# Kernel tuning notes

Measured on AMD Instinct MI355X. Metric: run time of the kernel, lower is better.

## Reference

```python
import jax, jax.numpy as jnp
import numpy as np

NUM_FRAMES = 16   # frames gathered per proposal (hardcoded 16 in source)
TOPK = 3          # get_max_score_timestamps uses topk=3


def setup_inputs() -> dict:
    key = jax.random.key(0)
    k0, k1, k2, k3, k4 = jax.random.split(key, 5)
    B, S, N, T, D = 64, 16, 256, 256, 500
    frames_feat = jax.random.normal(k0, (B, T, D), dtype=jnp.float32)
    duration = jax.random.uniform(k1, (B,), minval=30.0, maxval=120.0, dtype=jnp.float32)
    s = jax.random.uniform(k2, (B, S), minval=0.0, maxval=0.8, dtype=jnp.float32) * duration[:, None]
    length = jax.random.uniform(k3, (B, S), minval=0.05, maxval=0.2, dtype=jnp.float32) * duration[:, None]
    e = jnp.minimum(s + length, duration[:, None])
    props = jnp.stack([s, e], axis=-1)          # [B,S,2] (start,end) seconds
    y_t = props[:, :, None, :]                  # [B,S,1,2] gt timestamps
    scores = jax.random.uniform(k4, (B, S, 1, N, N), dtype=jnp.float32)
    return {"frames_feat": frames_feat, "props": props, "duration": duration,
            "y_t": y_t, "scores": scores}


def reference(frames_feat, props, duration, y_t, scores):
    B, T, D = frames_feat.shape
    S = props.shape[1]
    N = scores.shape[-1]

    # ---- _generate_proposals_feat: vectorized per-proposal frame gather ----
    s_fr = jnp.minimum((props[..., 0] / duration[:, None] * T).astype(jnp.int32), T - 1)  # [B,S]
    e_fr = jnp.minimum((props[..., 1] / duration[:, None] * T).astype(jnp.int32), T - 1)
    steps = jnp.arange(NUM_FRAMES, dtype=jnp.float32)
    # np.linspace(s, e, 16, endpoint=False) == s + k*(e-s)/16, then int cast + clamp
    lin = s_fr[..., None].astype(jnp.float32) + steps * (e_fr - s_fr)[..., None].astype(jnp.float32) / NUM_FRAMES
    idx = jnp.minimum(lin.astype(jnp.int32), T - 1)                       # [B,S,16]
    gathered = jnp.take_along_axis(frames_feat[:, None], idx[..., None], axis=2)  # [B,S,16,D]
    zero_prop = (props[..., 0] == 0) & (props[..., 1] == 0) & (duration[:, None] == 0)
    props_feats = jnp.where(zero_prop[..., None, None], 0.0, gathered).reshape(B * S, NUM_FRAMES, D)

    # ---- calculate_overlaps: IoU of all (s_i, e_j) clip pairs vs gt segment ----
    s_times = jnp.arange(N, dtype=jnp.float32) * duration[:, None] / N        # [B,N]
    e_times = jnp.arange(1, N + 1, dtype=jnp.float32) * duration[:, None] / N  # [B,N]
    gt_s = y_t[:, :, 0, 0]   # [B,S]
    gt_e = y_t[:, :, 0, 1]
    ps = s_times[:, None, :, None]                 # [B,1,N,1] pred start (row i)
    pe = e_times[:, None, None, :]                 # [B,1,1,N] pred end   (col j)
    gs = gt_s[:, :, None, None]
    ge = gt_e[:, :, None, None]
    inter = jnp.maximum(0.0, jnp.minimum(pe, ge) - jnp.maximum(ps, gs))
    union = jnp.maximum(0.0, jnp.maximum(pe, ge) - jnp.minimum(ps, gs))
    overlaps = inter / (union + 1e-6)              # [B,S,N,N]
    gt_zero = (gt_s == 0) & (gt_e == 0)
    overlaps = jnp.where(gt_zero[..., None, None], 0.0, overlaps)

    # ---- get_max_score_timestamps: batched top-3 over flattened NxN maps ----
    score_map = scores[:, :, 0]                    # [B,S,N,N]
    flat = score_map.reshape(B, S, N * N)
    top_vals, top_idx = jax.lax.top_k(flat, TOPK)  # [B,S,3]
    pos_i = (top_idx // N).astype(jnp.float32)
    pos_j = (top_idx % N).astype(jnp.float32)
    # target_size = NUM_SAMPLE_CLIPS // TARGET_STRIDE == N here
    ts = jnp.stack([pos_i, pos_j], axis=-1) / N * duration[:, None, None, None]  # [B,S,3,2]
    valid = (flat.sum(-1) > 0.001)[..., None]      # [B,S,1]
    max_scores = jnp.where(valid, top_vals, 0.0)
    max_timestamps = jnp.where(valid[..., None], ts, 0.0)

    return props_feats, overlaps, max_timestamps, max_scores
```

## Files before the change

kernel.cpp:

```cpp
#include <hip/hip_runtime.h>
#include <float.h>

typedef float f32x4 __attribute__((ext_vector_type(4)));

static constexpr long OUT0 = 0;
static constexpr long OUT1 = 8192000;
static constexpr long OUT2 = 75300864;
static constexpr long OUT3 = 75307008;

__global__ __launch_bounds__(256) void propfeat_kernel(
    const float* __restrict__ frames, const float* __restrict__ props,
    const float* __restrict__ duration, float* __restrict__ out) {
  int bs = blockIdx.x;
  int b = bs >> 4;
  float dur = duration[b];
  float p0 = props[bs * 2 + 0];
  float p1 = props[bs * 2 + 1];
  int s_fr = (int)(p0 / dur * 256.0f); if (s_fr > 255) s_fr = 255;
  int e_fr = (int)(p1 / dur * 256.0f); if (e_fr > 255) e_fr = 255;
  bool zp = (p0 == 0.0f) && (p1 == 0.0f) && (dur == 0.0f);
  float sf = (float)s_fr;
  float df = (float)(e_fr - s_fr);
  const f32x4* f4 = (const f32x4*)frames + (long)b * (256L * 125L);
  f32x4* o4 = (f32x4*)out + OUT0 / 4 + (long)bs * (16L * 125L);
  for (int k = threadIdx.x; k < 2000; k += 256) {
    int f = k / 125;
    int w = k - f * 125;
    float lin = sf + ((float)f * df) * (1.0f / 16.0f);
    int idx = (int)lin; if (idx > 255) idx = 255; if (idx < 0) idx = 0;
    f32x4 v = f4[(long)idx * 125 + w];
    if (zp) v = (f32x4){0.0f, 0.0f, 0.0f, 0.0f};
    __builtin_nontemporal_store(v, &o4[k]);
  }
}


__device__ __forceinline__ void insert_stream(float v, int id, float tv[3], int ti[3]) {
  if (v > tv[2]) {
    if (v > tv[0]) {
      tv[2] = tv[1]; ti[2] = ti[1];
      tv[1] = tv[0]; ti[1] = ti[0];
      tv[0] = v;     ti[0] = id;
    } else if (v > tv[1]) {
      tv[2] = tv[1]; ti[2] = ti[1];
      tv[1] = v;     ti[1] = id;
    } else {
      tv[2] = v;     ti[2] = id;
    }
  }
}

__device__ __forceinline__ void insert_merge(float v, int id, float tv[3], int ti[3]) {
  if (v > tv[2] || (v == tv[2] && id < ti[2])) {
    if (v > tv[0] || (v == tv[0] && id < ti[0])) {
      tv[2] = tv[1]; ti[2] = ti[1];
      tv[1] = tv[0]; ti[1] = ti[0];
      tv[0] = v;     ti[0] = id;
    } else if (v > tv[1] || (v == tv[1] && id < ti[1])) {
      tv[2] = tv[1]; ti[2] = ti[1];
      tv[1] = v;     ti[1] = id;
    } else {
      tv[2] = v;     ti[2] = id;
    }
  }
}

__global__ __launch_bounds__(512, 8) void ov_topk_kernel(
    const float* __restrict__ scores, const float* __restrict__ yt,
    const float* __restrict__ duration, float* __restrict__ out) {
  __shared__ float sv[1536];
  __shared__ int   si[1536];
  __shared__ float ssum[512];

  int bs = blockIdx.x;
  int b = bs >> 4;
  int tid = threadIdx.x;
  float dur = duration[b];
  float gs = yt[bs * 2 + 0];
  float ge = yt[bs * 2 + 1];
  bool gz = (gs == 0.0f) && (ge == 0.0f);
  const float inv256 = 1.0f / 256.0f;

  int j = (tid & 63) << 2;
  float pe1 = (float)(j + 1) * dur * inv256;
  float pe2 = (float)(j + 2) * dur * inv256;
  float pe3 = (float)(j + 3) * dur * inv256;
  float pe4 = (float)(j + 4) * dur * inv256;
  float mn1 = fminf(pe1, ge), mx1 = fmaxf(pe1, ge);
  float mn2 = fminf(pe2, ge), mx2 = fmaxf(pe2, ge);
  float mn3 = fminf(pe3, ge), mx3 = fmaxf(pe3, ge);
  float mn4 = fminf(pe4, ge), mx4 = fmaxf(pe4, ge);

  const f32x4* s4 = (const f32x4*)scores + (long)bs * 16384L;
  f32x4* o4 = (f32x4*)out + OUT1 / 4 + (long)bs * 16384L;

  float tv[3] = {-FLT_MAX, -FLT_MAX, -FLT_MAX};
  int   ti[3] = {0x7fffffff, 0x7fffffff, 0x7fffffff};
  float lsum = 0.0f;

#define OVROW(K)                                                          \
  {                                                                       \
    int i = (K) >> 6;                                                     \
    float ps = (float)i * dur * inv256;                                   \
    float pmg = fmaxf(ps, gs);                                            \
    float pmn = fminf(ps, gs);                                            \
    f32x4 ov;                                                             \
    ov.x = gz ? 0.0f : fmaxf(0.0f, mn1 - pmg) *                           \
                       __builtin_amdgcn_rcpf(fmaxf(0.0f, mx1 - pmn) + 1e-6f); \
    ov.y = gz ? 0.0f : fmaxf(0.0f, mn2 - pmg) *                           \
                       __builtin_amdgcn_rcpf(fmaxf(0.0f, mx2 - pmn) + 1e-6f); \
    ov.z = gz ? 0.0f : fmaxf(0.0f, mn3 - pmg) *                           \
                       __builtin_amdgcn_rcpf(fmaxf(0.0f, mx3 - pmn) + 1e-6f); \
    ov.w = gz ? 0.0f : fmaxf(0.0f, mn4 - pmg) *                           \
                       __builtin_amdgcn_rcpf(fmaxf(0.0f, mx4 - pmn) + 1e-6f); \
    __builtin_nontemporal_store(ov, &o4[K]);                              \
  }

#define TOPK4(SC, K)                                                      \
  {                                                                       \
    int fidx = (K) << 2;                                                  \
    insert_stream(SC.x, fidx + 0, tv, ti);                                \
    insert_stream(SC.y, fidx + 1, tv, ti);                                \
    insert_stream(SC.z, fidx + 2, tv, ti);                                \
    insert_stream(SC.w, fidx + 3, tv, ti);                                \
    lsum += SC.x + SC.y + SC.z + SC.w;                                    \
  }

  for (int it = 0; it < 32; it += 4) {
    int k0 = it * 512 + tid;
    int k1 = k0 + 512;
    int k2 = k0 + 1024;
    int k3 = k0 + 1536;
    f32x4 a = s4[k0];
    f32x4 c = s4[k1];
    f32x4 d = s4[k2];
    f32x4 e = s4[k3];
    OVROW(k0); TOPK4(a, k0);
    OVROW(k1); TOPK4(c, k1);
    OVROW(k2); TOPK4(d, k2);
    OVROW(k3); TOPK4(e, k3);
  }
#undef OVROW
#undef TOPK4

  ssum[tid] = lsum;
  sv[tid * 3 + 0] = tv[0]; si[tid * 3 + 0] = ti[0];
  sv[tid * 3 + 1] = tv[1]; si[tid * 3 + 1] = ti[1];
  sv[tid * 3 + 2] = tv[2]; si[tid * 3 + 2] = ti[2];
  __syncthreads();

  for (int sft = 256; sft > 0; sft >>= 1) {
    if (tid < sft) ssum[tid] += ssum[tid + sft];
    __syncthreads();
  }

  if (tid < 64) {
    float fv[3] = {-FLT_MAX, -FLT_MAX, -FLT_MAX};
    int   fi[3] = {0x7fffffff, 0x7fffffff, 0x7fffffff};
    for (int t = tid; t < 512; t += 64) {
      insert_merge(sv[t * 3 + 0], si[t * 3 + 0], fv, fi);
      insert_merge(sv[t * 3 + 1], si[t * 3 + 1], fv, fi);
      insert_merge(sv[t * 3 + 2], si[t * 3 + 2], fv, fi);
    }
    sv[tid * 3 + 0] = fv[0]; si[tid * 3 + 0] = fi[0];
    sv[tid * 3 + 1] = fv[1]; si[tid * 3 + 1] = fi[1];
    sv[tid * 3 + 2] = fv[2]; si[tid * 3 + 2] = fi[2];
  }
  __syncthreads();

  if (tid == 0) {
    float fv[3] = {-FLT_MAX, -FLT_MAX, -FLT_MAX};
    int   fi[3] = {0x7fffffff, 0x7fffffff, 0x7fffffff};
    for (int t = 0; t < 64; ++t) {
      insert_merge(sv[t * 3 + 0], si[t * 3 + 0], fv, fi);
      insert_merge(sv[t * 3 + 1], si[t * 3 + 1], fv, fi);
      insert_merge(sv[t * 3 + 2], si[t * 3 + 2], fv, fi);
    }
    float total = ssum[0];
    bool valid = total > 0.001f;
    float* o2 = out + OUT2 + (long)bs * 6;
    float* o3 = out + OUT3 + (long)bs * 3;
    for (int r = 0; r < 3; ++r) {
      float pi = (float)(fi[r] >> 8);
      float pj = (float)(fi[r] & 255);
      o3[r]         = valid ? fv[r] : 0.0f;
      o2[r * 2 + 0] = valid ? (pi * inv256) * dur : 0.0f;
      o2[r * 2 + 1] = valid ? (pj * inv256) * dur : 0.0f;
    }
  }
}

extern "C" void kernel_launch(void* const* d_in, const int* in_sizes, int n_in,
                              void* d_out, int out_size, void* d_ws, size_t ws_size,
                              hipStream_t stream) {
  const float* frames   = (const float*)d_in[0];
  const float* props    = (const float*)d_in[1];
  const float* duration = (const float*)d_in[2];
  const float* yt       = (const float*)d_in[3];
  const float* scores   = (const float*)d_in[4];
  float* out = (float*)d_out;

  hipLaunchKernelGGL(propfeat_kernel, dim3(1024), dim3(256), 0, stream,
                     frames, props, duration, out);
  hipLaunchKernelGGL(ov_topk_kernel, dim3(1024), dim3(512), 0, stream,
                     scores, yt, duration, out);
}
```

Baseline: 122.2 us.

## Fuse frame-gather and overlap/top-k kernels into one launch with wave-shuffle reductions

Merges the proposal-feature gather and the overlap/top-k kernels into a single launch, with odd blocks doing the gather and even blocks doing overlap plus top-3. The overlap blocks shrink from 512 to 256 threads, each handling twice as many rows. The shared-memory tree reductions for sum and top-3 are replaced by 64-lane xor-shuffle reductions followed by a small cross-wave merge. It also switches the first 384 proposals' score reads to nontemporal loads, which changes cache behaviour. The aim is to drop one launch and its tail, let both memory-bound phases overlap, and cut barrier and LDS traffic, at the cost of fewer threads per top-k block.

```diff
diff --git a/kernel.cpp b/kernel.cpp
--- a/kernel.cpp
+++ b/kernel.cpp
@@ -8,32 +8,20 @@
 static constexpr long OUT2 = 75300864;
 static constexpr long OUT3 = 75307008;
 
-__global__ __launch_bounds__(256) void propfeat_kernel(
-    const float* __restrict__ frames, const float* __restrict__ props,
-    const float* __restrict__ duration, float* __restrict__ out) {
-  int bs = blockIdx.x;
-  int b = bs >> 4;
-  float dur = duration[b];
-  float p0 = props[bs * 2 + 0];
-  float p1 = props[bs * 2 + 1];
-  int s_fr = (int)(p0 / dur * 256.0f); if (s_fr > 255) s_fr = 255;
-  int e_fr = (int)(p1 / dur * 256.0f); if (e_fr > 255) e_fr = 255;
-  bool zp = (p0 == 0.0f) && (p1 == 0.0f) && (dur == 0.0f);
-  float sf = (float)s_fr;
-  float df = (float)(e_fr - s_fr);
-  const f32x4* f4 = (const f32x4*)frames + (long)b * (256L * 125L);
-  f32x4* o4 = (f32x4*)out + OUT0 / 4 + (long)bs * (16L * 125L);
-  for (int k = threadIdx.x; k < 2000; k += 256) {
-    int f = k / 125;
-    int w = k - f * 125;
-    float lin = sf + ((float)f * df) * (1.0f / 16.0f);
-    int idx = (int)lin; if (idx > 255) idx = 255; if (idx < 0) idx = 0;
-    f32x4 v = f4[(long)idx * 125 + w];
-    if (zp) v = (f32x4){0.0f, 0.0f, 0.0f, 0.0f};
-    __builtin_nontemporal_store(v, &o4[k]);
-  }
-}
-
+__device__ __forceinline__ void insert_merge(float v, int id, float tv[3], int ti[3]) {
+  if (v > tv[2] || (v == tv[2] && id < ti[2])) {
+    if (v > tv[0] || (v == tv[0] && id < ti[0])) {
+      tv[2] = tv[1]; ti[2] = ti[1];
+      tv[1] = tv[0]; ti[1] = ti[0];
+      tv[0] = v;     ti[0] = id;
+    } else if (v > tv[1] || (v == tv[1] && id < ti[1])) {
+      tv[2] = tv[1]; ti[2] = ti[1];
+      tv[1] = v;     ti[1] = id;
+    } else {
+      tv[2] = v;     ti[2] = id;
+    }
+  }
+}
 
 __device__ __forceinline__ void insert_stream(float v, int id, float tv[3], int ti[3]) {
   if (v > tv[2]) {
@@ -50,32 +38,60 @@
   }
 }
 
-__device__ __forceinline__ void insert_merge(float v, int id, float tv[3], int ti[3]) {
-  if (v > tv[2] || (v == tv[2] && id < ti[2])) {
-    if (v > tv[0] || (v == tv[0] && id < ti[0])) {
-      tv[2] = tv[1]; ti[2] = ti[1];
-      tv[1] = tv[0]; ti[1] = ti[0];
-      tv[0] = v;     ti[0] = id;
-    } else if (v > tv[1] || (v == tv[1] && id < ti[1])) {
-      tv[2] = tv[1]; ti[2] = ti[1];
-      tv[1] = v;     ti[1] = id;
-    } else {
-      tv[2] = v;     ti[2] = id;
-    }
-  }
-}
-
-__global__ __launch_bounds__(512, 8) void ov_topk_kernel(
-    const float* __restrict__ scores, const float* __restrict__ yt,
-    const float* __restrict__ duration, float* __restrict__ out) {
-  __shared__ float sv[1536];
-  __shared__ int   si[1536];
-  __shared__ float ssum[512];
-
-  int bs = blockIdx.x;
+__device__ __forceinline__ void wave_merge3(float tv[3], int ti[3]) {
+  #pragma unroll
+  for (int m = 1; m < 64; m <<= 1) {
+    float v0 = __shfl_xor(tv[0], m, 64); int i0 = __shfl_xor(ti[0], m, 64);
+    float v1 = __shfl_xor(tv[1], m, 64); int i1 = __shfl_xor(ti[1], m, 64);
+    float v2 = __shfl_xor(tv[2], m, 64); int i2 = __shfl_xor(ti[2], m, 64);
+    insert_merge(v0, i0, tv, ti);
+    insert_merge(v1, i1, tv, ti);
+    insert_merge(v2, i2, tv, ti);
+  }
+}
+
+__device__ __forceinline__ float wave_sum(float x) {
+  #pragma unroll
+  for (int m = 1; m < 64; m <<= 1) x += __shfl_xor(x, m, 64);
+  return x;
+}
+
+__global__ __launch_bounds__(256) void fused_kernel(
+    const float* __restrict__ frames, const float* __restrict__ props,
+    const float* __restrict__ duration, const float* __restrict__ yt,
+    const float* __restrict__ scores, float* __restrict__ out) {
+  int gb = blockIdx.x;
+  int bs = gb >> 1;
   int b = bs >> 4;
   int tid = threadIdx.x;
   float dur = duration[b];
+
+  if (gb & 1) {
+    float p0 = props[bs * 2 + 0];
+    float p1 = props[bs * 2 + 1];
+    int s_fr = (int)(p0 / dur * 256.0f); if (s_fr > 255) s_fr = 255;
+    int e_fr = (int)(p1 / dur * 256.0f); if (e_fr > 255) e_fr = 255;
+    bool zp = (p0 == 0.0f) && (p1 == 0.0f) && (dur == 0.0f);
+    float sf = (float)s_fr;
+    float df = (float)(e_fr - s_fr);
+    const f32x4* f4 = (const f32x4*)frames + (long)b * (256L * 125L);
+    f32x4* o4 = (f32x4*)out + OUT0 / 4 + (long)bs * (16L * 125L);
+    for (int k = tid; k < 2000; k += 256) {
+      int f = k / 125;
+      int w = k - f * 125;
+      float lin = sf + ((float)f * df) * (1.0f / 16.0f);
+      int idx = (int)lin; if (idx > 255) idx = 255; if (idx < 0) idx = 0;
+      f32x4 v = f4[(long)idx * 125 + w];
+      if (zp) v = (f32x4){0.0f, 0.0f, 0.0f, 0.0f};
+      __builtin_nontemporal_store(v, &o4[k]);
+    }
+    return;
+  }
+
+  __shared__ float swv[12];
+  __shared__ int   swi[12];
+  __shared__ float swsum[4];
+
   float gs = yt[bs * 2 + 0];
   float ge = yt[bs * 2 + 1];
   bool gz = (gs == 0.0f) && (ge == 0.0f);
@@ -126,60 +142,52 @@
     lsum += SC.x + SC.y + SC.z + SC.w;                                    \
   }
 
-  for (int it = 0; it < 32; it += 4) {
-    int k0 = it * 512 + tid;
-    int k1 = k0 + 512;
-    int k2 = k0 + 1024;
-    int k3 = k0 + 1536;
-    f32x4 a = s4[k0];
-    f32x4 c = s4[k1];
-    f32x4 d = s4[k2];
-    f32x4 e = s4[k3];
-    OVROW(k0); TOPK4(a, k0);
-    OVROW(k1); TOPK4(c, k1);
-    OVROW(k2); TOPK4(d, k2);
-    OVROW(k3); TOPK4(e, k3);
-  }
+#define MAINLOOP(LOADF)                                                   \
+  for (int it = 0; it < 64; it += 4) {                                    \
+    int k0 = it * 256 + tid;                                              \
+    int k1 = k0 + 256;                                                    \
+    int k2 = k0 + 512;                                                    \
+    int k3 = k0 + 768;                                                    \
+    f32x4 a = LOADF(&s4[k0]);                                             \
+    f32x4 c = LOADF(&s4[k1]);                                             \
+    f32x4 d = LOADF(&s4[k2]);                                             \
+    f32x4 e = LOADF(&s4[k3]);                                             \
+    OVROW(k0); TOPK4(a, k0);                                              \
+    OVROW(k1); TOPK4(c, k1);                                              \
+    OVROW(k2); TOPK4(d, k2);                                              \
+    OVROW(k3); TOPK4(e, k3);                                              \
+  }
+
+#define NTLOAD(P)  __builtin_nontemporal_load(P)
+#define NLOAD(P)   (*(P))
+  if (bs < 384) { MAINLOOP(NTLOAD) } else { MAINLOOP(NLOAD) }
+#undef NTLOAD
+#undef NLOAD
+#undef MAINLOOP
 #undef OVROW
 #undef TOPK4
 
-  ssum[tid] = lsum;
-  sv[tid * 3 + 0] = tv[0]; si[tid * 3 + 0] = ti[0];
-  sv[tid * 3 + 1] = tv[1]; si[tid * 3 + 1] = ti[1];
-  sv[tid * 3 + 2] = tv[2]; si[tid * 3 + 2] = ti[2];
-  __syncthreads();
-
-  for (int sft = 256; sft > 0; sft >>= 1) {
-    if (tid < sft) ssum[tid] += ssum[tid + sft];
-    __syncthreads();
-  }
-
-  if (tid < 64) {
-    float fv[3] = {-FLT_MAX, -FLT_MAX, -FLT_MAX};
-    int   fi[3] = {0x7fffffff, 0x7fffffff, 0x7fffffff};
-    for (int t = tid; t < 512; t += 64) {
-      insert_merge(sv[t * 3 + 0], si[t * 3 + 0], fv, fi);
-      insert_merge(sv[t * 3 + 1], si[t * 3 + 1], fv, fi);
-      insert_merge(sv[t * 3 + 2], si[t * 3 + 2], fv, fi);
-    }
-    sv[tid * 3 + 0] = fv[0]; si[tid * 3 + 0] = fi[0];
-    sv[tid * 3 + 1] = fv[1]; si[tid * 3 + 1] = fi[1];
-    sv[tid * 3 + 2] = fv[2]; si[tid * 3 + 2] = fi[2];
+  wave_merge3(tv, ti);
+  lsum = wave_sum(lsum);
+  int wave = tid >> 6;
+  if ((tid & 63) == 0) {
+    swv[wave * 3 + 0] = tv[0]; swi[wave * 3 + 0] = ti[0];
+    swv[wave * 3 + 1] = tv[1]; swi[wave * 3 + 1] = ti[1];
+    swv[wave * 3 + 2] = tv[2]; swi[wave * 3 + 2] = ti[2];
+    swsum[wave] = lsum;
   }
   __syncthreads();
 
   if (tid == 0) {
     float fv[3] = {-FLT_MAX, -FLT_MAX, -FLT_MAX};
     int   fi[3] = {0x7fffffff, 0x7fffffff, 0x7fffffff};
-    for (int t = 0; t < 64; ++t) {
-      insert_merge(sv[t * 3 + 0], si[t * 3 + 0], fv, fi);
-      insert_merge(sv[t * 3 + 1], si[t * 3 + 1], fv, fi);
-      insert_merge(sv[t * 3 + 2], si[t * 3 + 2], fv, fi);
-    }
-    float total = ssum[0];
+    #pragma unroll
+    for (int t = 0; t < 12; ++t) insert_merge(swv[t], swi[t], fv, fi);
+    float total = swsum[0] + swsum[1] + swsum[2] + swsum[3];
     bool valid = total > 0.001f;
     float* o2 = out + OUT2 + (long)bs * 6;
     float* o3 = out + OUT3 + (long)bs * 3;
+    #pragma unroll
     for (int r = 0; r < 3; ++r) {
       float pi = (float)(fi[r] >> 8);
       float pj = (float)(fi[r] & 255);
@@ -200,8 +208,6 @@
   const float* scores   = (const float*)d_in[4];
   float* out = (float*)d_out;
 
-  hipLaunchKernelGGL(propfeat_kernel, dim3(1024), dim3(256), 0, stream,
-                     frames, props, duration, out);
-  hipLaunchKernelGGL(ov_topk_kernel, dim3(1024), dim3(512), 0, stream,
-                     scores, yt, duration, out);
-}
+  hipLaunchKernelGGL(fused_kernel, dim3(2048), dim3(256), 0, stream,
+                     frames, props, duration, yt, scores, out);
+}
```

New measurement: 133.1 us. 1.09x slower.
